# Performance work log

Measured on AMD Instinct MI355X. Metric: run time of the kernel, lower is better.

## Reference

```python
import jax, jax.numpy as jnp
import numpy as np

N, E, G = 50000, 800000, 128
IN_DIM, HID, HEADS, OUT_DIM = 256, 64, 4, 10
HC = HID * HEADS  # 256
NEG_SLOPE = 0.2


def _gat_layer(x, src, dst, W, att_src, att_dst, bias):
    # x: [N, F_in]; W: [F_in, H*C]; att_*: [H, C]; bias: [H*C]
    n = x.shape[0]
    h = (x @ W).reshape(n, HEADS, HID)                      # [N,H,C]
    a_src = jnp.einsum('nhc,hc->nh', h, att_src)            # [N,H]
    a_dst = jnp.einsum('nhc,hc->nh', h, att_dst)            # [N,H]
    e = a_src[src] + a_dst[dst]                             # [E,H]
    e = jax.nn.leaky_relu(e, NEG_SLOPE)
    # segment softmax over incoming edges of each dst node
    m = jax.ops.segment_max(e, dst, num_segments=n)         # [N,H]
    ex = jnp.exp(e - m[dst])
    denom = jax.ops.segment_sum(ex, dst, num_segments=n)    # [N,H]
    alpha = ex / (denom[dst] + 1e-16)                       # [E,H]
    msg = h[src] * alpha[:, :, None]                        # [E,H,C]
    out = jax.ops.segment_sum(msg, dst, num_segments=n)     # [N,H,C]
    return out.reshape(n, HC) + bias


def setup_inputs() -> dict:
    key = jax.random.key(0)
    ks = jax.random.split(key, 16)
    x = jax.random.normal(ks[0], (N, IN_DIM), dtype=jnp.float32)
    edge_index = jax.random.randint(ks[1], (2, E), 0, N, dtype=jnp.int64)
    edge_weight = jax.random.uniform(ks[2], (E,), dtype=jnp.float32)
    batch = jnp.sort(jax.random.randint(ks[3], (N,), 0, G, dtype=jnp.int64))
    s = 0.05
    W1 = jax.random.normal(ks[4], (IN_DIM, HC), dtype=jnp.float32) * s
    att_src1 = jax.random.normal(ks[5], (HEADS, HID), dtype=jnp.float32) * s
    att_dst1 = jax.random.normal(ks[6], (HEADS, HID), dtype=jnp.float32) * s
    b1 = jnp.zeros((HC,), dtype=jnp.float32)
    W2 = jax.random.normal(ks[7], (HC, HC), dtype=jnp.float32) * s
    att_src2 = jax.random.normal(ks[8], (HEADS, HID), dtype=jnp.float32) * s
    att_dst2 = jax.random.normal(ks[9], (HEADS, HID), dtype=jnp.float32) * s
    b2 = jnp.zeros((HC,), dtype=jnp.float32)
    Wf = jax.random.normal(ks[10], (HC, OUT_DIM), dtype=jnp.float32) * s
    bf = jnp.zeros((OUT_DIM,), dtype=jnp.float32)
    return dict(x=x, edge_index=edge_index, edge_weight=edge_weight, batch=batch,
                W1=W1, att_src1=att_src1, att_dst1=att_dst1, b1=b1,
                W2=W2, att_src2=att_src2, att_dst2=att_dst2, b2=b2,
                Wf=Wf, bf=bf)


def reference(x, edge_index, edge_weight, batch,
              W1, att_src1, att_dst1, b1,
              W2, att_src2, att_dst2, b2,
              Wf, bf):
    n = x.shape[0]
    # add self loops (add_self_loops=True in GATConv)
    loop = jnp.arange(n, dtype=edge_index.dtype)
    ei = jnp.concatenate([edge_index, jnp.stack([loop, loop])], axis=1)
    src, dst = ei[0], ei[1]
    h = jax.nn.relu(_gat_layer(x, src, dst, W1, att_src1, att_dst1, b1))
    h = jax.nn.relu(_gat_layer(h, src, dst, W2, att_src2, att_dst2, b2))
    # global mean pool per graph
    counts = jax.ops.segment_sum(jnp.ones((n,), dtype=h.dtype), batch, num_segments=G)
    pooled = jax.ops.segment_sum(h, batch, num_segments=G) / jnp.maximum(counts, 1.0)[:, None]
    out = pooled @ Wf + bf
    return out, pooled
```

## Files before the change

### kernel.cpp

```cpp
#include <hip/hip_runtime.h>
#include <math.h>

#define HEADS 4
#define HID 64
#define HC 256
#define NEG_SLOPE 0.2f
#define GG 128

typedef __attribute__((ext_vector_type(8))) short short8;
typedef __attribute__((ext_vector_type(4))) float floatx4;
typedef unsigned short ush;

__device__ __forceinline__ ush f2bf(float f) {
  unsigned u = __float_as_uint(f);
  unsigned r = (u + 0x7FFFu + ((u >> 16) & 1u)) >> 16;
  return (ush)r;
}
__device__ __forceinline__ float bf2f(ush h) {
  return __uint_as_float(((unsigned)h) << 16);
}

__global__ void hist_kernel(const int* __restrict__ ei, int* counts, int E, int n) {
  int i = blockIdx.x * 256 + threadIdx.x;
  if (i >= E + n) return;
  int d = (i < E) ? ei[E + i] : (i - E);
  atomicAdd(&counts[d], 1);
}

__global__ __launch_bounds__(256) void scan_pass1(const int* __restrict__ counts,
                                                  int* __restrict__ bsums, int n) {
  int t = threadIdx.x;
  int i0 = blockIdx.x * 1024 + t * 4;
  int s = 0;
  if (i0 + 3 < n) {
    int4 v = *(const int4*)&counts[i0];
    s = v.x + v.y + v.z + v.w;
  } else {
#pragma unroll
    for (int k = 0; k < 4; ++k)
      if (i0 + k < n) s += counts[i0 + k];
  }
#pragma unroll
  for (int o = 1; o < 64; o <<= 1) s += __shfl_xor(s, o, 64);
  __shared__ int ws[4];
  if ((t & 63) == 0) ws[t >> 6] = s;
  __syncthreads();
  if (t == 0) bsums[blockIdx.x] = ws[0] + ws[1] + ws[2] + ws[3];
}

__global__ __launch_bounds__(256) void scan_pass2(int* __restrict__ bsums,
                                                  int* __restrict__ row_ptr, int nb, int n) {
  __shared__ int sh[256];
  int t = threadIdx.x;
  int v = (t < nb) ? bsums[t] : 0;
  sh[t] = v;
  __syncthreads();
  for (int off = 1; off < 256; off <<= 1) {
    int u = (t >= off) ? sh[t - off] : 0;
    __syncthreads();
    sh[t] += u;
    __syncthreads();
  }
  if (t < nb) bsums[t] = sh[t] - v;
  if (t == 255) row_ptr[n] = sh[255];
}

__global__ __launch_bounds__(256) void scan_pass3(const int* __restrict__ counts,
                                                  const int* __restrict__ bsums,
                                                  int* __restrict__ row_ptr,
                                                  int* __restrict__ cursor, int n) {
  int t = threadIdx.x;
  int i0 = blockIdx.x * 1024 + t * 4;
  int c0 = 0, c1 = 0, c2 = 0, c3 = 0;
  bool full = (i0 + 3 < n);
  if (full) {
    int4 v = *(const int4*)&counts[i0];
    c0 = v.x; c1 = v.y; c2 = v.z; c3 = v.w;
  } else {
    if (i0 + 0 < n) c0 = counts[i0 + 0];
    if (i0 + 1 < n) c1 = counts[i0 + 1];
    if (i0 + 2 < n) c2 = counts[i0 + 2];
    if (i0 + 3 < n) c3 = counts[i0 + 3];
  }
  int ts = c0 + c1 + c2 + c3;
  __shared__ int sh[256];
  sh[t] = ts;
  __syncthreads();
  for (int off = 1; off < 256; off <<= 1) {
    int u = (t >= off) ? sh[t - off] : 0;
    __syncthreads();
    sh[t] += u;
    __syncthreads();
  }
  int run = bsums[blockIdx.x] + sh[t] - ts;
  int r0 = run, r1 = run + c0, r2 = r1 + c1, r3 = r2 + c2;
  if (full) {
    *(int4*)&row_ptr[i0] = make_int4(r0, r1, r2, r3);
    *(int4*)&cursor[i0] = make_int4(r0, r1, r2, r3);
  } else {
    if (i0 + 0 < n) { row_ptr[i0 + 0] = r0; cursor[i0 + 0] = r0; }
    if (i0 + 1 < n) { row_ptr[i0 + 1] = r1; cursor[i0 + 1] = r1; }
    if (i0 + 2 < n) { row_ptr[i0 + 2] = r2; cursor[i0 + 2] = r2; }
    if (i0 + 3 < n) { row_ptr[i0 + 3] = r3; cursor[i0 + 3] = r3; }
  }
}

__global__ void scatter_kernel(const int* __restrict__ ei, int* cursor, int* srcs, int E, int n) {
  int i = blockIdx.x * 256 + threadIdx.x;
  if (i >= E + n) return;
  int s, d;
  if (i < E) { s = ei[i]; d = ei[E + i]; }
  else       { s = i - E; d = s; }
  int pos = atomicAdd(&cursor[d], 1);
  srcs[pos] = s;
}

__global__ __launch_bounds__(256) void splitA_kernel(const float* __restrict__ A,
                                                     ush* __restrict__ Ah,
                                                     ush* __restrict__ Al, int total) {
  int i0 = (blockIdx.x * 256 + threadIdx.x) * 4;
  if (i0 + 3 < total) {
    float4 v = *(const float4*)&A[i0];
    ushort4 h = make_ushort4(f2bf(v.x), f2bf(v.y), f2bf(v.z), f2bf(v.w));
    ushort4 l = make_ushort4(f2bf(v.x - bf2f(h.x)), f2bf(v.y - bf2f(h.y)),
                             f2bf(v.z - bf2f(h.z)), f2bf(v.w - bf2f(h.w)));
    *(ushort4*)&Ah[i0] = h;
    *(ushort4*)&Al[i0] = l;
  } else {
    for (int k = 0; k < 4 && i0 + k < total; ++k) {
      float v = A[i0 + k];
      ush h = f2bf(v);
      Ah[i0 + k] = h;
      Al[i0 + k] = f2bf(v - bf2f(h));
    }
  }
}

__global__ void convertB_kernel(const float* __restrict__ W1, const float* __restrict__ W2,
                                ush* __restrict__ Bth1, ush* __restrict__ Btl1,
                                ush* __restrict__ Bth2, ush* __restrict__ Btl2) {
  int k = blockIdx.x, n = threadIdx.x;
  const float* B = blockIdx.y ? W2 : W1;
  ush* th = blockIdx.y ? Bth2 : Bth1;
  ush* tl = blockIdx.y ? Btl2 : Btl1;
  float v = B[k * HC + n];
  ush h = f2bf(v);
  ush l = f2bf(v - bf2f(h));
  th[n * HC + k] = h;
  tl[n * HC + k] = l;
}

#define LDA 40
__global__ __launch_bounds__(256) void gemm_kernel(
    const ush* __restrict__ Ah, const ush* __restrict__ Al,
    const ush* __restrict__ Bth, const ush* __restrict__ Btl,
    const float* __restrict__ att_src, const float* __restrict__ att_dst,
    ush* __restrict__ Cb, float* __restrict__ asrc_o, float* __restrict__ adst_o, int M) {
  __shared__ ush sAh[128 * LDA];
  __shared__ ush sAl[128 * LDA];
  __shared__ ush sBh[128 * LDA];
  __shared__ ush sBl[128 * LDA];

  int t = threadIdx.x;
  int lane = t & 63, wave = t >> 6;
  int wm = wave >> 1, wn = wave & 1;
  int q = lane >> 4, mrow = lane & 15;
  int r0 = blockIdx.y * 128;
  int c0 = blockIdx.x * 128;
  const int4 zero4 = make_int4(0, 0, 0, 0);

  int row0 = t >> 2, seg0 = t & 3;
  int row1 = (t + 256) >> 2, seg1 = (t + 256) & 3;
  bool v0 = (r0 + row0) < M, v1 = (r0 + row1) < M;

  const ush* Ag0 = Ah + (size_t)(r0 + row0) * HC + seg0 * 8;
  const ush* Ag1 = Ah + (size_t)(r0 + row1) * HC + seg1 * 8;
  const ush* Al0 = Al + (size_t)(r0 + row0) * HC + seg0 * 8;
  const ush* Al1 = Al + (size_t)(r0 + row1) * HC + seg1 * 8;
  const ush* Bg0 = Bth + (size_t)(c0 + row0) * HC + seg0 * 8;
  const ush* Bg1 = Bth + (size_t)(c0 + row1) * HC + seg1 * 8;
  const ush* Bl0 = Btl + (size_t)(c0 + row0) * HC + seg0 * 8;
  const ush* Bl1 = Btl + (size_t)(c0 + row1) * HC + seg1 * 8;

  int4 pAh0, pAh1, pAl0, pAl1, pBh0, pBh1, pBl0, pBl1;
  pAh0 = v0 ? *(const int4*)(Ag0) : zero4;
  pAh1 = v1 ? *(const int4*)(Ag1) : zero4;
  pAl0 = v0 ? *(const int4*)(Al0) : zero4;
  pAl1 = v1 ? *(const int4*)(Al1) : zero4;
  pBh0 = *(const int4*)(Bg0);
  pBh1 = *(const int4*)(Bg1);
  pBl0 = *(const int4*)(Bl0);
  pBl1 = *(const int4*)(Bl1);

  floatx4 acc[4][4];
#pragma unroll
  for (int i = 0; i < 4; ++i)
#pragma unroll
    for (int j = 0; j < 4; ++j) acc[i][j] = (floatx4)(0.0f);

  for (int k0 = 0; k0 < HC; k0 += 32) {
    *(int4*)&sAh[row0 * LDA + seg0 * 8] = pAh0;
    *(int4*)&sAh[row1 * LDA + seg1 * 8] = pAh1;
    *(int4*)&sAl[row0 * LDA + seg0 * 8] = pAl0;
    *(int4*)&sAl[row1 * LDA + seg1 * 8] = pAl1;
    *(int4*)&sBh[row0 * LDA + seg0 * 8] = pBh0;
    *(int4*)&sBh[row1 * LDA + seg1 * 8] = pBh1;
    *(int4*)&sBl[row0 * LDA + seg0 * 8] = pBl0;
    *(int4*)&sBl[row1 * LDA + seg1 * 8] = pBl1;
    __syncthreads();

    int kn = k0 + 32;
    if (kn < HC) {
      pAh0 = v0 ? *(const int4*)(Ag0 + kn) : zero4;
      pAh1 = v1 ? *(const int4*)(Ag1 + kn) : zero4;
      pAl0 = v0 ? *(const int4*)(Al0 + kn) : zero4;
      pAl1 = v1 ? *(const int4*)(Al1 + kn) : zero4;
      pBh0 = *(const int4*)(Bg0 + kn);
      pBh1 = *(const int4*)(Bg1 + kn);
      pBl0 = *(const int4*)(Bl0 + kn);
      pBl1 = *(const int4*)(Bl1 + kn);
    }

    short8 ah[4], al[4], bh[4], bl[4];
#pragma unroll
    for (int i = 0; i < 4; ++i) {
      int ar = (wm * 64 + i * 16 + mrow) * LDA + q * 8;
      int br = (wn * 64 + i * 16 + mrow) * LDA + q * 8;
      ah[i] = *(short8*)&sAh[ar];
      al[i] = *(short8*)&sAl[ar];
      bh[i] = *(short8*)&sBh[br];
      bl[i] = *(short8*)&sBl[br];
    }
#pragma unroll
    for (int i = 0; i < 4; ++i)
#pragma unroll
      for (int j = 0; j < 4; ++j) {
        acc[i][j] = __builtin_amdgcn_mfma_f32_16x16x32_bf16(ah[i], bh[j], acc[i][j], 0, 0, 0);
        acc[i][j] = __builtin_amdgcn_mfma_f32_16x16x32_bf16(ah[i], bl[j], acc[i][j], 0, 0, 0);
        acc[i][j] = __builtin_amdgcn_mfma_f32_16x16x32_bf16(al[i], bh[j], acc[i][j], 0, 0, 0);
      }
    __syncthreads();
  }

  int hd = (c0 >> 6) + wn;
  float aS[4], aD[4];
#pragma unroll
  for (int j = 0; j < 4; ++j) {
    aS[j] = att_src[hd * 64 + j * 16 + mrow];
    aD[j] = att_dst[hd * 64 + j * 16 + mrow];
  }
#pragma unroll
  for (int i = 0; i < 4; ++i) {
#pragma unroll
    for (int r = 0; r < 4; ++r) {
      float ps = acc[i][0][r] * aS[0] + acc[i][1][r] * aS[1] +
                 acc[i][2][r] * aS[2] + acc[i][3][r] * aS[3];
      float pd = acc[i][0][r] * aD[0] + acc[i][1][r] * aD[1] +
                 acc[i][2][r] * aD[2] + acc[i][3][r] * aD[3];
#pragma unroll
      for (int o = 1; o < 16; o <<= 1) {
        ps += __shfl_xor(ps, o, 64);
        pd += __shfl_xor(pd, o, 64);
      }
      int grow = r0 + wm * 64 + i * 16 + q * 4 + r;
      if (mrow == 0 && grow < M) {
        asrc_o[grow * HEADS + hd] = ps;
        adst_o[grow * HEADS + hd] = pd;
      }
    }
  }

#pragma unroll
  for (int i = 0; i < 4; ++i) {
#pragma unroll
    for (int j = 0; j < 4; ++j) {
      int col = c0 + wn * 64 + j * 16 + mrow;
#pragma unroll
      for (int r = 0; r < 4; ++r) {
        int grow = r0 + wm * 64 + i * 16 + q * 4 + r;
        if (grow < M) Cb[(size_t)grow * HC + col] = f2bf(acc[i][j][r]);
      }
    }
  }
}

__device__ __forceinline__ float lrelu(float x) { return x > 0.f ? x : NEG_SLOPE * x; }

__global__ __launch_bounds__(256) void aggregate_kernel(
    const ush* __restrict__ hbf, const float* __restrict__ asrc,
    const float* __restrict__ adst, const int* __restrict__ row_ptr,
    const int* __restrict__ srcs, const float* __restrict__ bias,
    float* __restrict__ outf, ush* __restrict__ outh, ush* __restrict__ outl, int N) {
  __shared__ float s_alpha[4][64 * 4];
  __shared__ int s_src[4][64];

  int wave = threadIdx.x >> 6;
  int lane = threadIdx.x & 63;
  int node = blockIdx.x * 4 + wave;
  if (node >= N) return;

  int begin = row_ptr[node];
  int end = row_ptr[node + 1];
  int deg = end - begin;
  int nb = deg < 64 ? deg : 64;

  const float4* asrc4 = (const float4*)asrc;
  float4 ad = ((const float4*)adst)[node];

  const float NEGINF = -3.402823466e38f;
  int s0 = 0;
  float4 e0 = make_float4(NEGINF, NEGINF, NEGINF, NEGINF);
  if (lane < nb) {
    s0 = srcs[begin + lane];
    float4 a = asrc4[s0];
    e0.x = lrelu(a.x + ad.x);
    e0.y = lrelu(a.y + ad.y);
    e0.z = lrelu(a.z + ad.z);
    e0.w = lrelu(a.w + ad.w);
  }
  float m0 = e0.x, m1 = e0.y, m2 = e0.z, m3 = e0.w;
  for (int base = 64; base < deg; base += 64) {
    int idx = base + lane;
    if (idx < deg) {
      int s = srcs[begin + idx];
      float4 a = asrc4[s];
      m0 = fmaxf(m0, lrelu(a.x + ad.x));
      m1 = fmaxf(m1, lrelu(a.y + ad.y));
      m2 = fmaxf(m2, lrelu(a.z + ad.z));
      m3 = fmaxf(m3, lrelu(a.w + ad.w));
    }
  }
#pragma unroll
  for (int o = 1; o < 64; o <<= 1) {
    m0 = fmaxf(m0, __shfl_xor(m0, o, 64));
    m1 = fmaxf(m1, __shfl_xor(m1, o, 64));
    m2 = fmaxf(m2, __shfl_xor(m2, o, 64));
    m3 = fmaxf(m3, __shfl_xor(m3, o, 64));
  }
  float ex0 = (lane < nb) ? __expf(e0.x - m0) : 0.f;
  float ex1 = (lane < nb) ? __expf(e0.y - m1) : 0.f;
  float ex2 = (lane < nb) ? __expf(e0.z - m2) : 0.f;
  float ex3 = (lane < nb) ? __expf(e0.w - m3) : 0.f;
  float d0 = ex0, d1 = ex1, d2 = ex2, d3 = ex3;
  for (int base = 64; base < deg; base += 64) {
    int idx = base + lane;
    if (idx < deg) {
      int s = srcs[begin + idx];
      float4 a = asrc4[s];
      d0 += __expf(lrelu(a.x + ad.x) - m0);
      d1 += __expf(lrelu(a.y + ad.y) - m1);
      d2 += __expf(lrelu(a.z + ad.z) - m2);
      d3 += __expf(lrelu(a.w + ad.w) - m3);
    }
  }
#pragma unroll
  for (int o = 1; o < 64; o <<= 1) {
    d0 += __shfl_xor(d0, o, 64);
    d1 += __shfl_xor(d1, o, 64);
    d2 += __shfl_xor(d2, o, 64);
    d3 += __shfl_xor(d3, o, 64);
  }
  float r0 = 1.0f / (d0 + 1e-16f);
  float r1 = 1.0f / (d1 + 1e-16f);
  float r2 = 1.0f / (d2 + 1e-16f);
  float r3 = 1.0f / (d3 + 1e-16f);

  *(float4*)&s_alpha[wave][lane * 4] = make_float4(ex0 * r0, ex1 * r1, ex2 * r2, ex3 * r3);
  s_src[wave][lane] = s0;

  int head = lane >> 4;
  float mh = (head == 0) ? m0 : (head == 1) ? m1 : (head == 2) ? m2 : m3;
  float rdh = (head == 0) ? r0 : (head == 1) ? r1 : (head == 2) ? r2 : r3;
  float adh = (head == 0) ? ad.x : (head == 1) ? ad.y : (head == 2) ? ad.z : ad.w;

  const ushort4* hb4 = (const ushort4*)hbf;
  float4 accA = make_float4(0.f, 0.f, 0.f, 0.f);
  float4 accB = accA, accC = accA, accD = accA;
  int i = 0;
  for (; i + 4 <= nb; i += 4) {
    int sa = s_src[wave][i];
    int sb = s_src[wave][i + 1];
    int sc = s_src[wave][i + 2];
    int sd = s_src[wave][i + 3];
    float aa = s_alpha[wave][i * 4 + head];
    float ab = s_alpha[wave][(i + 1) * 4 + head];
    float ac = s_alpha[wave][(i + 2) * 4 + head];
    float ad_ = s_alpha[wave][(i + 3) * 4 + head];
    ushort4 u0 = hb4[(size_t)sa * 64 + lane];
    ushort4 u1 = hb4[(size_t)sb * 64 + lane];
    ushort4 u2 = hb4[(size_t)sc * 64 + lane];
    ushort4 u3 = hb4[(size_t)sd * 64 + lane];
    accA.x += aa * bf2f(u0.x); accA.y += aa * bf2f(u0.y);
    accA.z += aa * bf2f(u0.z); accA.w += aa * bf2f(u0.w);
    accB.x += ab * bf2f(u1.x); accB.y += ab * bf2f(u1.y);
    accB.z += ab * bf2f(u1.z); accB.w += ab * bf2f(u1.w);
    accC.x += ac * bf2f(u2.x); accC.y += ac * bf2f(u2.y);
    accC.z += ac * bf2f(u2.z); accC.w += ac * bf2f(u2.w);
    accD.x += ad_ * bf2f(u3.x); accD.y += ad_ * bf2f(u3.y);
    accD.z += ad_ * bf2f(u3.z); accD.w += ad_ * bf2f(u3.w);
  }
  for (; i < nb; ++i) {
    int s = s_src[wave][i];
    float a = s_alpha[wave][i * 4 + head];
    ushort4 u = hb4[(size_t)s * 64 + lane];
    accA.x += a * bf2f(u.x); accA.y += a * bf2f(u.y);
    accA.z += a * bf2f(u.z); accA.w += a * bf2f(u.w);
  }
  for (int i2 = 64; i2 < deg; ++i2) {
    int s = srcs[begin + i2];
    float ash = asrc[s * HEADS + head];
    float a = __expf(lrelu(ash + adh) - mh) * rdh;
    ushort4 u = hb4[(size_t)s * 64 + lane];
    accA.x += a * bf2f(u.x); accA.y += a * bf2f(u.y);
    accA.z += a * bf2f(u.z); accA.w += a * bf2f(u.w);
  }

  float4 acc;
  acc.x = (accA.x + accB.x) + (accC.x + accD.x);
  acc.y = (accA.y + accB.y) + (accC.y + accD.y);
  acc.z = (accA.z + accB.z) + (accC.z + accD.z);
  acc.w = (accA.w + accB.w) + (accC.w + accD.w);
  float4 bv = ((const float4*)bias)[lane];
  float4 o;
  o.x = fmaxf(acc.x + bv.x, 0.f);
  o.y = fmaxf(acc.y + bv.y, 0.f);
  o.z = fmaxf(acc.z + bv.z, 0.f);
  o.w = fmaxf(acc.w + bv.w, 0.f);

  if (outf) {
    ((float4*)outf)[(size_t)node * 64 + lane] = o;
  } else {
    ushort4 h = make_ushort4(f2bf(o.x), f2bf(o.y), f2bf(o.z), f2bf(o.w));
    ((ushort4*)outh)[(size_t)node * 64 + lane] = h;
    if (outl) {
      ushort4 l = make_ushort4(f2bf(o.x - bf2f(h.x)), f2bf(o.y - bf2f(h.y)),
                               f2bf(o.z - bf2f(h.z)), f2bf(o.w - bf2f(h.w)));
      ((ushort4*)outl)[(size_t)node * 64 + lane] = l;
    }
  }
}

__device__ __forceinline__ int lower_bound_i(const int* a, int n, int key) {
  int lo = 0, hi = n;
  while (lo < hi) {
    int mid = (lo + hi) >> 1;
    if (a[mid] < key) lo = mid + 1; else hi = mid;
  }
  return lo;
}

__global__ __launch_bounds__(256) void pool_kernel(const ush* __restrict__ h2,
                                                   const int* __restrict__ batch,
                                                   float* __restrict__ pws,
                                                   int* __restrict__ cnts, int n) {
  int g = blockIdx.x, part = blockIdx.y;
  int wave = threadIdx.x >> 6, lane = threadIdx.x & 63;
  int lo = lower_bound_i(batch, n, g);
  int hi = lower_bound_i(batch, n, g + 1);
  const ushort4* h4 = (const ushort4*)h2;
  float4 acc = make_float4(0.f, 0.f, 0.f, 0.f);
  for (int i = lo + part * 4 + wave; i < hi; i += 16) {
    ushort4 u = h4[(size_t)i * 64 + lane];
    acc.x += bf2f(u.x); acc.y += bf2f(u.y);
    acc.z += bf2f(u.z); acc.w += bf2f(u.w);
  }
  __shared__ float4 red[4][64];
  red[wave][lane] = acc;
  __syncthreads();
  if (wave == 0) {
    float4 a0 = red[0][lane], a1 = red[1][lane], a2 = red[2][lane], a3 = red[3][lane];
    float4 o;
    o.x = (a0.x + a1.x) + (a2.x + a3.x);
    o.y = (a0.y + a1.y) + (a2.y + a3.y);
    o.z = (a0.z + a1.z) + (a2.z + a3.z);
    o.w = (a0.w + a1.w) + (a2.w + a3.w);
    ((float4*)pws)[(size_t)(g * 4 + part) * 64 + lane] = o;
  }
  if (part == 0 && threadIdx.x == 0) cnts[g] = hi - lo;
}

__global__ void final_kernel(const float* __restrict__ pws, const int* __restrict__ cnts,
                             const float* __restrict__ Wf, const float* __restrict__ bf,
                             float* __restrict__ pooled_out, float* __restrict__ out) {
  int g = blockIdx.x, t = threadIdx.x;
  float s = pws[(size_t)(g * 4 + 0) * 256 + t] + pws[(size_t)(g * 4 + 1) * 256 + t] +
            pws[(size_t)(g * 4 + 2) * 256 + t] + pws[(size_t)(g * 4 + 3) * 256 + t];
  float inv = 1.0f / fmaxf((float)cnts[g], 1.0f);
  float pv = s * inv;
  pooled_out[g * HC + t] = pv;
  __shared__ float p[HC];
  p[t] = pv;
  __syncthreads();
  if (t < 10) {
    float acc = bf[t];
    for (int c = 0; c < HC; ++c) acc += p[c] * Wf[c * 10 + t];
    out[g * 10 + t] = acc;
  }
}

extern "C" void kernel_launch(void* const* d_in, const int* in_sizes, int n_in,
                              void* d_out, int out_size, void* d_ws, size_t ws_size,
                              hipStream_t stream) {
  const float* x    = (const float*)d_in[0];
  const int*   ei   = (const int*)d_in[1];
  const int*   batch = (const int*)d_in[3];
  const float* W1   = (const float*)d_in[4];
  const float* as1  = (const float*)d_in[5];
  const float* ad1  = (const float*)d_in[6];
  const float* b1   = (const float*)d_in[7];
  const float* W2   = (const float*)d_in[8];
  const float* as2  = (const float*)d_in[9];
  const float* ad2  = (const float*)d_in[10];
  const float* b2   = (const float*)d_in[11];
  const float* Wf   = (const float*)d_in[12];
  const float* bf   = (const float*)d_in[13];
  float* out = (float*)d_out;

  const int N = in_sizes[0] / HC;
  const int E = in_sizes[1] / 2;

  char* base = (char*)d_ws;
  size_t off = 0;
  auto alloc = [&](size_t bytes) {
    char* p = base + off;
    off = (off + bytes + 255) & ~(size_t)255;
    return p;
  };
  ush* xh = (ush*)alloc((size_t)N * HC * 2);
  ush* xl = (ush*)alloc((size_t)N * HC * 2);
  ush* hbf = (ush*)alloc((size_t)N * HC * 2);
  float* asrc = (float*)alloc((size_t)N * HEADS * 4);
  float* adst = (float*)alloc((size_t)N * HEADS * 4);
  int* counts = (int*)alloc((size_t)N * 4);
  int* row_ptr = (int*)alloc((size_t)(N + 1) * 4);
  int* cursor = (int*)alloc((size_t)N * 4);
  int* srcs = (int*)alloc((size_t)(E + N) * 4);
  int* bsums = (int*)alloc(((N + 1023) / 1024) * 4);
  ush* Bth1 = (ush*)alloc((size_t)HC * HC * 2);
  ush* Btl1 = (ush*)alloc((size_t)HC * HC * 2);
  ush* Bth2 = (ush*)alloc((size_t)HC * HC * 2);
  ush* Btl2 = (ush*)alloc((size_t)HC * HC * 2);
  float* pws = (float*)alloc((size_t)GG * 4 * HC * 4);
  int* cnts = (int*)alloc((size_t)GG * 4);

  int nb = (N + 1023) / 1024;

  hipMemsetAsync(counts, 0, (size_t)N * 4, stream);
  hist_kernel<<<(E + N + 255) / 256, 256, 0, stream>>>(ei, counts, E, N);
  scan_pass1<<<nb, 256, 0, stream>>>(counts, bsums, N);
  scan_pass2<<<1, 256, 0, stream>>>(bsums, row_ptr, nb, N);
  scan_pass3<<<nb, 256, 0, stream>>>(counts, bsums, row_ptr, cursor, N);
  scatter_kernel<<<(E + N + 255) / 256, 256, 0, stream>>>(ei, cursor, srcs, E, N);

  dim3 cbgrid(HC, 2);
  convertB_kernel<<<cbgrid, HC, 0, stream>>>(W1, W2, Bth1, Btl1, Bth2, Btl2);
  splitA_kernel<<<(N * HC / 4 + 255) / 256, 256, 0, stream>>>(x, xh, xl, N * HC);

  dim3 ggrid(2, (N + 127) / 128);
  int agg_blocks = (N + 3) / 4;

  gemm_kernel<<<ggrid, 256, 0, stream>>>(xh, xl, Bth1, Btl1, as1, ad1, hbf, asrc, adst, N);
  aggregate_kernel<<<agg_blocks, 256, 0, stream>>>(hbf, asrc, adst, row_ptr, srcs, b1,
                                                   nullptr, xh, xl, N);

  gemm_kernel<<<ggrid, 256, 0, stream>>>(xh, xl, Bth2, Btl2, as2, ad2, hbf, asrc, adst, N);
  aggregate_kernel<<<agg_blocks, 256, 0, stream>>>(hbf, asrc, adst, row_ptr, srcs, b2,
                                                   nullptr, xh, nullptr, N);

  dim3 pgrid(GG, 4);
  pool_kernel<<<pgrid, 256, 0, stream>>>(xh, batch, pws, cnts, N);
  final_kernel<<<GG, 256, 0, stream>>>(pws, cnts, Wf, bf, out + GG * 10, out);
}
```

Baseline: 471.8 us.

## Fuse fp32 input split into GEMM and widen aggregate gathers to 16 bytes

The separate splitA pass is removed. The first GEMM now reads the fp32 input directly and splits it into bf16 hi/lo parts while staging into shared memory, which avoids writing and rereading the split arrays. The aggregate kernel now has each half-wave gather 16-byte short8 rows for alternating edges and combines the halves with a cross-half shuffle, instead of 8-byte loads across the full wave with four accumulators. The trade-off is extra conversion arithmetic inside the GEMM (repeated for each of the two column blocks) and half the lanes idle during the output store.

Result: slower. 508.0 us (+7.7%).

```diff
diff --git a/kernel.cpp b/kernel.cpp
--- a/kernel.cpp
+++ b/kernel.cpp
@@ -115,27 +115,6 @@
   srcs[pos] = s;
 }
 
-__global__ __launch_bounds__(256) void splitA_kernel(const float* __restrict__ A,
-                                                     ush* __restrict__ Ah,
-                                                     ush* __restrict__ Al, int total) {
-  int i0 = (blockIdx.x * 256 + threadIdx.x) * 4;
-  if (i0 + 3 < total) {
-    float4 v = *(const float4*)&A[i0];
-    ushort4 h = make_ushort4(f2bf(v.x), f2bf(v.y), f2bf(v.z), f2bf(v.w));
-    ushort4 l = make_ushort4(f2bf(v.x - bf2f(h.x)), f2bf(v.y - bf2f(h.y)),
-                             f2bf(v.z - bf2f(h.z)), f2bf(v.w - bf2f(h.w)));
-    *(ushort4*)&Ah[i0] = h;
-    *(ushort4*)&Al[i0] = l;
-  } else {
-    for (int k = 0; k < 4 && i0 + k < total; ++k) {
-      float v = A[i0 + k];
-      ush h = f2bf(v);
-      Ah[i0 + k] = h;
-      Al[i0 + k] = f2bf(v - bf2f(h));
-    }
-  }
-}
-
 __global__ void convertB_kernel(const float* __restrict__ W1, const float* __restrict__ W2,
                                 ush* __restrict__ Bth1, ush* __restrict__ Btl1,
                                 ush* __restrict__ Bth2, ush* __restrict__ Btl2) {
@@ -150,8 +129,16 @@
   tl[n * HC + k] = l;
 }
 
+__device__ __forceinline__ void cvt4(float4 v, ushort4* h, ushort4* l) {
+  ushort4 hh = make_ushort4(f2bf(v.x), f2bf(v.y), f2bf(v.z), f2bf(v.w));
+  *h = hh;
+  *l = make_ushort4(f2bf(v.x - bf2f(hh.x)), f2bf(v.y - bf2f(hh.y)),
+                    f2bf(v.z - bf2f(hh.z)), f2bf(v.w - bf2f(hh.w)));
+}
+
 #define LDA 40
 __global__ __launch_bounds__(256) void gemm_kernel(
+    const float* __restrict__ Axf,
     const ush* __restrict__ Ah, const ush* __restrict__ Al,
     const ush* __restrict__ Bth, const ush* __restrict__ Btl,
     const float* __restrict__ att_src, const float* __restrict__ att_dst,
@@ -168,6 +155,8 @@
   int r0 = blockIdx.y * 128;
   int c0 = blockIdx.x * 128;
   const int4 zero4 = make_int4(0, 0, 0, 0);
+  const float4 zf4 = make_float4(0.f, 0.f, 0.f, 0.f);
+  bool f32 = (Axf != nullptr);
 
   int row0 = t >> 2, seg0 = t & 3;
   int row1 = (t + 256) >> 2, seg1 = (t + 256) & 3;
@@ -177,16 +166,26 @@
   const ush* Ag1 = Ah + (size_t)(r0 + row1) * HC + seg1 * 8;
   const ush* Al0 = Al + (size_t)(r0 + row0) * HC + seg0 * 8;
   const ush* Al1 = Al + (size_t)(r0 + row1) * HC + seg1 * 8;
+  const float* X0 = Axf + (size_t)(r0 + row0) * HC + seg0 * 8;
+  const float* X1 = Axf + (size_t)(r0 + row1) * HC + seg1 * 8;
   const ush* Bg0 = Bth + (size_t)(c0 + row0) * HC + seg0 * 8;
   const ush* Bg1 = Bth + (size_t)(c0 + row1) * HC + seg1 * 8;
   const ush* Bl0 = Btl + (size_t)(c0 + row0) * HC + seg0 * 8;
   const ush* Bl1 = Btl + (size_t)(c0 + row1) * HC + seg1 * 8;
 
   int4 pAh0, pAh1, pAl0, pAl1, pBh0, pBh1, pBl0, pBl1;
-  pAh0 = v0 ? *(const int4*)(Ag0) : zero4;
-  pAh1 = v1 ? *(const int4*)(Ag1) : zero4;
-  pAl0 = v0 ? *(const int4*)(Al0) : zero4;
-  pAl1 = v1 ? *(const int4*)(Al1) : zero4;
+  float4 pX0a, pX0b, pX1a, pX1b;
+  if (f32) {
+    pX0a = v0 ? *(const float4*)(X0) : zf4;
+    pX0b = v0 ? *(const float4*)(X0 + 4) : zf4;
+    pX1a = v1 ? *(const float4*)(X1) : zf4;
+    pX1b = v1 ? *(const float4*)(X1 + 4) : zf4;
+  } else {
+    pAh0 = v0 ? *(const int4*)(Ag0) : zero4;
+    pAh1 = v1 ? *(const int4*)(Ag1) : zero4;
+    pAl0 = v0 ? *(const int4*)(Al0) : zero4;
+    pAl1 = v1 ? *(const int4*)(Al1) : zero4;
+  }
   pBh0 = *(const int4*)(Bg0);
   pBh1 = *(const int4*)(Bg1);
   pBl0 = *(const int4*)(Bl0);
@@ -199,10 +198,26 @@
     for (int j = 0; j < 4; ++j) acc[i][j] = (floatx4)(0.0f);
 
   for (int k0 = 0; k0 < HC; k0 += 32) {
-    *(int4*)&sAh[row0 * LDA + seg0 * 8] = pAh0;
-    *(int4*)&sAh[row1 * LDA + seg1 * 8] = pAh1;
-    *(int4*)&sAl[row0 * LDA + seg0 * 8] = pAl0;
-    *(int4*)&sAl[row1 * LDA + seg1 * 8] = pAl1;
+    if (f32) {
+      ushort4 h, l;
+      cvt4(pX0a, &h, &l);
+      *(ushort4*)&sAh[row0 * LDA + seg0 * 8] = h;
+      *(ushort4*)&sAl[row0 * LDA + seg0 * 8] = l;
+      cvt4(pX0b, &h, &l);
+      *(ushort4*)&sAh[row0 * LDA + seg0 * 8 + 4] = h;
+      *(ushort4*)&sAl[row0 * LDA + seg0 * 8 + 4] = l;
+      cvt4(pX1a, &h, &l);
+      *(ushort4*)&sAh[row1 * LDA + seg1 * 8] = h;
+      *(ushort4*)&sAl[row1 * LDA + seg1 * 8] = l;
+      cvt4(pX1b, &h, &l);
+      *(ushort4*)&sAh[row1 * LDA + seg1 * 8 + 4] = h;
+      *(ushort4*)&sAl[row1 * LDA + seg1 * 8 + 4] = l;
+    } else {
+      *(int4*)&sAh[row0 * LDA + seg0 * 8] = pAh0;
+      *(int4*)&sAh[row1 * LDA + seg1 * 8] = pAh1;
+      *(int4*)&sAl[row0 * LDA + seg0 * 8] = pAl0;
+      *(int4*)&sAl[row1 * LDA + seg1 * 8] = pAl1;
+    }
     *(int4*)&sBh[row0 * LDA + seg0 * 8] = pBh0;
     *(int4*)&sBh[row1 * LDA + seg1 * 8] = pBh1;
     *(int4*)&sBl[row0 * LDA + seg0 * 8] = pBl0;
@@ -211,10 +226,17 @@
 
     int kn = k0 + 32;
     if (kn < HC) {
-      pAh0 = v0 ? *(const int4*)(Ag0 + kn) : zero4;
-      pAh1 = v1 ? *(const int4*)(Ag1 + kn) : zero4;
-      pAl0 = v0 ? *(const int4*)(Al0 + kn) : zero4;
-      pAl1 = v1 ? *(const int4*)(Al1 + kn) : zero4;
+      if (f32) {
+        pX0a = v0 ? *(const float4*)(X0 + kn) : zf4;
+        pX0b = v0 ? *(const float4*)(X0 + kn + 4) : zf4;
+        pX1a = v1 ? *(const float4*)(X1 + kn) : zf4;
+        pX1b = v1 ? *(const float4*)(X1 + kn + 4) : zf4;
+      } else {
+        pAh0 = v0 ? *(const int4*)(Ag0 + kn) : zero4;
+        pAh1 = v1 ? *(const int4*)(Ag1 + kn) : zero4;
+        pAl0 = v0 ? *(const int4*)(Al0 + kn) : zero4;
+        pAl1 = v1 ? *(const int4*)(Al1 + kn) : zero4;
+      }
       pBh0 = *(const int4*)(Bg0 + kn);
       pBh1 = *(const int4*)(Bg1 + kn);
       pBl0 = *(const int4*)(Bl0 + kn);
@@ -368,74 +390,70 @@
   *(float4*)&s_alpha[wave][lane * 4] = make_float4(ex0 * r0, ex1 * r1, ex2 * r2, ex3 * r3);
   s_src[wave][lane] = s0;
 
-  int head = lane >> 4;
-  float mh = (head == 0) ? m0 : (head == 1) ? m1 : (head == 2) ? m2 : m3;
-  float rdh = (head == 0) ? r0 : (head == 1) ? r1 : (head == 2) ? r2 : r3;
-  float adh = (head == 0) ? ad.x : (head == 1) ? ad.y : (head == 2) ? ad.z : ad.w;
-
-  const ushort4* hb4 = (const ushort4*)hbf;
-  float4 accA = make_float4(0.f, 0.f, 0.f, 0.f);
-  float4 accB = accA, accC = accA, accD = accA;
-  int i = 0;
-  for (; i + 4 <= nb; i += 4) {
-    int sa = s_src[wave][i];
-    int sb = s_src[wave][i + 1];
-    int sc = s_src[wave][i + 2];
-    int sd = s_src[wave][i + 3];
-    float aa = s_alpha[wave][i * 4 + head];
-    float ab = s_alpha[wave][(i + 1) * 4 + head];
-    float ac = s_alpha[wave][(i + 2) * 4 + head];
-    float ad_ = s_alpha[wave][(i + 3) * 4 + head];
-    ushort4 u0 = hb4[(size_t)sa * 64 + lane];
-    ushort4 u1 = hb4[(size_t)sb * 64 + lane];
-    ushort4 u2 = hb4[(size_t)sc * 64 + lane];
-    ushort4 u3 = hb4[(size_t)sd * 64 + lane];
-    accA.x += aa * bf2f(u0.x); accA.y += aa * bf2f(u0.y);
-    accA.z += aa * bf2f(u0.z); accA.w += aa * bf2f(u0.w);
-    accB.x += ab * bf2f(u1.x); accB.y += ab * bf2f(u1.y);
-    accB.z += ab * bf2f(u1.z); accB.w += ab * bf2f(u1.w);
-    accC.x += ac * bf2f(u2.x); accC.y += ac * bf2f(u2.y);
-    accC.z += ac * bf2f(u2.z); accC.w += ac * bf2f(u2.w);
-    accD.x += ad_ * bf2f(u3.x); accD.y += ad_ * bf2f(u3.y);
-    accD.z += ad_ * bf2f(u3.z); accD.w += ad_ * bf2f(u3.w);
-  }
-  for (; i < nb; ++i) {
+  int half = lane >> 5;
+  int hl = lane & 31;
+  int headh = hl >> 3;
+  float mh = (headh == 0) ? m0 : (headh == 1) ? m1 : (headh == 2) ? m2 : m3;
+  float rdh = (headh == 0) ? r0 : (headh == 1) ? r1 : (headh == 2) ? r2 : r3;
+  float adh = (headh == 0) ? ad.x : (headh == 1) ? ad.y : (headh == 2) ? ad.z : ad.w;
+
+  const short8* hb8 = (const short8*)hbf;
+  float acc[8];
+#pragma unroll
+  for (int k = 0; k < 8; ++k) acc[k] = 0.f;
+
+  for (int i = half; i < nb; i += 2) {
     int s = s_src[wave][i];
-    float a = s_alpha[wave][i * 4 + head];
-    ushort4 u = hb4[(size_t)s * 64 + lane];
-    accA.x += a * bf2f(u.x); accA.y += a * bf2f(u.y);
-    accA.z += a * bf2f(u.z); accA.w += a * bf2f(u.w);
-  }
-  for (int i2 = 64; i2 < deg; ++i2) {
+    float a = s_alpha[wave][i * 4 + headh];
+    short8 u = hb8[(size_t)s * 32 + hl];
+#pragma unroll
+    for (int k = 0; k < 8; ++k) acc[k] += a * bf2f((ush)u[k]);
+  }
+  for (int i2 = 64 + half; i2 < deg; i2 += 2) {
     int s = srcs[begin + i2];
-    float ash = asrc[s * HEADS + head];
+    float ash = asrc[s * HEADS + headh];
     float a = __expf(lrelu(ash + adh) - mh) * rdh;
-    ushort4 u = hb4[(size_t)s * 64 + lane];
-    accA.x += a * bf2f(u.x); accA.y += a * bf2f(u.y);
-    accA.z += a * bf2f(u.z); accA.w += a * bf2f(u.w);
-  }
-
-  float4 acc;
-  acc.x = (accA.x + accB.x) + (accC.x + accD.x);
-  acc.y = (accA.y + accB.y) + (accC.y + accD.y);
-  acc.z = (accA.z + accB.z) + (accC.z + accD.z);
-  acc.w = (accA.w + accB.w) + (accC.w + accD.w);
-  float4 bv = ((const float4*)bias)[lane];
-  float4 o;
-  o.x = fmaxf(acc.x + bv.x, 0.f);
-  o.y = fmaxf(acc.y + bv.y, 0.f);
-  o.z = fmaxf(acc.z + bv.z, 0.f);
-  o.w = fmaxf(acc.w + bv.w, 0.f);
-
-  if (outf) {
-    ((float4*)outf)[(size_t)node * 64 + lane] = o;
-  } else {
-    ushort4 h = make_ushort4(f2bf(o.x), f2bf(o.y), f2bf(o.z), f2bf(o.w));
-    ((ushort4*)outh)[(size_t)node * 64 + lane] = h;
-    if (outl) {
-      ushort4 l = make_ushort4(f2bf(o.x - bf2f(h.x)), f2bf(o.y - bf2f(h.y)),
-                               f2bf(o.z - bf2f(h.z)), f2bf(o.w - bf2f(h.w)));
-      ((ushort4*)outl)[(size_t)node * 64 + lane] = l;
+    short8 u = hb8[(size_t)s * 32 + hl];
+#pragma unroll
+    for (int k = 0; k < 8; ++k) acc[k] += a * bf2f((ush)u[k]);
+  }
+
+#pragma unroll
+  for (int k = 0; k < 8; ++k) acc[k] += __shfl_xor(acc[k], 32, 64);
+
+  if (half == 0) {
+    float4 bv0 = ((const float4*)bias)[hl * 2];
+    float4 bv1 = ((const float4*)bias)[hl * 2 + 1];
+    float o0 = fmaxf(acc[0] + bv0.x, 0.f);
+    float o1 = fmaxf(acc[1] + bv0.y, 0.f);
+    float o2 = fmaxf(acc[2] + bv0.z, 0.f);
+    float o3 = fmaxf(acc[3] + bv0.w, 0.f);
+    float o4 = fmaxf(acc[4] + bv1.x, 0.f);
+    float o5 = fmaxf(acc[5] + bv1.y, 0.f);
+    float o6 = fmaxf(acc[6] + bv1.z, 0.f);
+    float o7 = fmaxf(acc[7] + bv1.w, 0.f);
+    if (outf) {
+      ((float4*)outf)[(size_t)node * 64 + hl * 2] = make_float4(o0, o1, o2, o3);
+      ((float4*)outf)[(size_t)node * 64 + hl * 2 + 1] = make_float4(o4, o5, o6, o7);
+    } else {
+      ush h0 = f2bf(o0), h1 = f2bf(o1), h2 = f2bf(o2), h3 = f2bf(o3);
+      ush h4 = f2bf(o4), h5 = f2bf(o5), h6 = f2bf(o6), h7 = f2bf(o7);
+      short8 hv;
+      hv[0] = (short)h0; hv[1] = (short)h1; hv[2] = (short)h2; hv[3] = (short)h3;
+      hv[4] = (short)h4; hv[5] = (short)h5; hv[6] = (short)h6; hv[7] = (short)h7;
+      *(short8*)&outh[(size_t)node * HC + hl * 8] = hv;
+      if (outl) {
+        short8 lv;
+        lv[0] = (short)f2bf(o0 - bf2f(h0));
+        lv[1] = (short)f2bf(o1 - bf2f(h1));
+        lv[2] = (short)f2bf(o2 - bf2f(h2));
+        lv[3] = (short)f2bf(o3 - bf2f(h3));
+        lv[4] = (short)f2bf(o4 - bf2f(h4));
+        lv[5] = (short)f2bf(o5 - bf2f(h5));
+        lv[6] = (short)f2bf(o6 - bf2f(h6));
+        lv[7] = (short)f2bf(o7 - bf2f(h7));
+        *(short8*)&outl[(size_t)node * HC + hl * 8] = lv;
+      }
     }
   }
 }
@@ -554,16 +572,17 @@
 
   dim3 cbgrid(HC, 2);
   convertB_kernel<<<cbgrid, HC, 0, stream>>>(W1, W2, Bth1, Btl1, Bth2, Btl2);
-  splitA_kernel<<<(N * HC / 4 + 255) / 256, 256, 0, stream>>>(x, xh, xl, N * HC);
 
   dim3 ggrid(2, (N + 127) / 128);
   int agg_blocks = (N + 3) / 4;
 
-  gemm_kernel<<<ggrid, 256, 0, stream>>>(xh, xl, Bth1, Btl1, as1, ad1, hbf, asrc, adst, N);
+  gemm_kernel<<<ggrid, 256, 0, stream>>>(x, nullptr, nullptr, Bth1, Btl1, as1, ad1,
+                                         hbf, asrc, adst, N);
   aggregate_kernel<<<agg_blocks, 256, 0, stream>>>(hbf, asrc, adst, row_ptr, srcs, b1,
                                                    nullptr, xh, xl, N);
 
-  gemm_kernel<<<ggrid, 256, 0, stream>>>(xh, xl, Bth2, Btl2, as2, ad2, hbf, asrc, adst, N);
+  gemm_kernel<<<ggrid, 256, 0, stream>>>(nullptr, xh, xl, Bth2, Btl2, as2, ad2,
+                                         hbf, asrc, adst, N);
   aggregate_kernel<<<agg_blocks, 256, 0, stream>>>(hbf, asrc, adst, row_ptr, srcs, b2,
                                                    nullptr, xh, nullptr, N);
 
```
